# Kernel optimization log

Measured on AMD Instinct MI355X. Metric: run time of the kernel, lower is better.

## Reference

```python
import jax, jax.numpy as jnp
import numpy as np

H = 768  # sparse grid height
W = 768  # sparse grid width
N = 200000  # active sites
CIN = 256
CB = 64


def setup_inputs() -> dict:
    key = jax.random.key(0)
    ks = jax.random.split(key, 11)
    rng = np.random.default_rng(0)
    # unique active-site linear coordinates on the HxW grid
    coords = jnp.asarray(np.sort(rng.choice(H * W, N, replace=False)).astype(np.int64))
    feats = jax.random.normal(ks[0], (N, CIN), jnp.float32)
    w1 = jax.random.normal(ks[1], (CIN, CB), jnp.float32) / np.float32(np.sqrt(CIN))
    w2 = jax.random.normal(ks[2], (9, CB, CB), jnp.float32) / np.float32(np.sqrt(9 * CB))
    w3 = jax.random.normal(ks[3], (CB, CIN), jnp.float32) / np.float32(np.sqrt(CB))
    s1 = jax.random.uniform(ks[4], (CB,), jnp.float32, 0.5, 1.5)
    b1 = jax.random.normal(ks[5], (CB,), jnp.float32) * 0.1
    s2 = jax.random.uniform(ks[6], (CB,), jnp.float32, 0.5, 1.5)
    b2 = jax.random.normal(ks[7], (CB,), jnp.float32) * 0.1
    s3 = jax.random.uniform(ks[8], (CIN,), jnp.float32, 0.5, 1.5)
    b3 = jax.random.normal(ks[9], (CIN,), jnp.float32) * 0.1
    return dict(feats=feats, coords=coords, w1=w1, w2=w2, w3=w3,
                s1=s1, b1=b1, s2=s2, b2=b2, s3=s3, b3=b3)


def sparse_conv3x3(feats, coords, w2):
    # active-site sparse 3x3 conv: gather valid neighbors, matmul per tap, accumulate
    idx_map = jnp.full((H * W,), -1, jnp.int32).at[coords].set(
        jnp.arange(N, dtype=jnp.int32))
    y, x = coords // W, coords % W
    out = jnp.zeros((N, w2.shape[2]), feats.dtype)
    k = 0
    for dy in (-1, 0, 1):
        for dx in (-1, 0, 1):
            ny, nx = y + dy, x + dx
            inb = (ny >= 0) & (ny < H) & (nx >= 0) & (nx < W)
            lin = jnp.clip(ny, 0, H - 1) * W + jnp.clip(nx, 0, W - 1)
            r = idx_map[lin]
            ok = inb & (r >= 0)
            g = jnp.where(ok[:, None], feats[jnp.maximum(r, 0)], 0.0)
            out = out + g @ w2[k]
            k += 1
    return out


def reference(feats, coords, w1, w2, w3, s1, b1, s2, b2, s3, b3):
    identity = feats
    out = jax.nn.relu((feats @ w1) * s1 + b1)            # conv1 1x1 + bn1 + relu
    out = jax.nn.relu(sparse_conv3x3(out, coords, w2) * s2 + b2)  # conv2 3x3 + bn2 + relu
    out = (out @ w3) * s3 + b3                            # conv3 1x1 + bn3
    return jax.nn.relu(out + identity)                    # residual + relu
```

## Files before the change

### kernel.cpp

```cpp
#include <hip/hip_runtime.h>
#include <hip/hip_bf16.h>
#include <stdint.h>

#define HH 768
#define WW 768
#define NN 200000
#define CI 256
#define CB 64

typedef __attribute__((ext_vector_type(8))) __bf16 bf16x8;
typedef __attribute__((ext_vector_type(4))) float f32x4;
typedef __attribute__((ext_vector_type(4))) unsigned short u16x4;

__device__ inline unsigned short f2bf(float f) {
    union { float f; unsigned int i; } v; v.f = f;
    unsigned int r = v.i + 0x7FFF + ((v.i >> 16) & 1);
    return (unsigned short)(r >> 16);
}
__device__ inline f32x4 mfma16(bf16x8 a, bf16x8 b, f32x4 c) {
    return __builtin_amdgcn_mfma_f32_16x16x32_bf16(a, b, c, 0, 0, 0);
}
__device__ inline bf16x8 ldfrag(const unsigned short* p) {
    return *(const bf16x8*)p;
}
__device__ inline bf16x8 ldfrag_f32(const float* p) {
    float4 f0 = *(const float4*)(p);
    float4 f1 = *(const float4*)(p + 4);
    bf16x8 a;
    a[0] = (__bf16)f0.x; a[1] = (__bf16)f0.y; a[2] = (__bf16)f0.z; a[3] = (__bf16)f0.w;
    a[4] = (__bf16)f1.x; a[5] = (__bf16)f1.y; a[6] = (__bf16)f1.z; a[7] = (__bf16)f1.w;
    return a;
}


__global__ void k_scatter(const int* __restrict__ coords, int* __restrict__ idx_map) {
    int i = blockIdx.x * 256 + threadIdx.x;
    if (i < NN) idx_map[coords[i]] = i;
}

__global__ void k_prepw(const float* __restrict__ w1,
                        const float* __restrict__ w2,
                        const float* __restrict__ w3,
                        unsigned short* __restrict__ w1t,
                        unsigned short* __restrict__ w2t,
                        unsigned short* __restrict__ w3t) {
    int tid = blockIdx.x * 256 + threadIdx.x;
    int stride = gridDim.x * 256;
    for (int i = tid; i < CI * CB; i += stride) {
        int k = i / CB, n = i % CB;
        w1t[n * CI + k] = f2bf(w1[i]);
    }
    for (int i = tid; i < 9 * CB * CB; i += stride) {
        int t = i / (CB * CB), rem = i % (CB * CB);
        int k = rem / CB, n = rem % CB;
        w2t[t * CB * CB + n * CB + k] = f2bf(w2[i]);
    }
    for (int i = tid; i < CB * CI; i += stride) {
        int k = i / CI, n = i % CI;
        w3t[n * CB + k] = f2bf(w3[i]);
    }
}


__global__ __launch_bounds__(256, 4) void k_gemm1(const float* __restrict__ feats,
                                                  const unsigned short* __restrict__ w1t,
                                                  const float* __restrict__ s1,
                                                  const float* __restrict__ b1,
                                                  unsigned short* __restrict__ out1) {
    const int wave = threadIdx.x >> 6;
    const int lane = threadIdx.x & 63;
    const int m = lane & 15;
    const int quad = lane >> 4;
    const int row0 = blockIdx.x * 128 + wave * 32;
    if (row0 >= NN) return;

    f32x4 acc[2][4];
#pragma unroll
    for (int rt = 0; rt < 2; ++rt)
#pragma unroll
        for (int ct = 0; ct < 4; ++ct) acc[rt][ct] = (f32x4){0.f, 0.f, 0.f, 0.f};

#pragma unroll
    for (int ks = 0; ks < 8; ++ks) {
        bf16x8 f[2];
#pragma unroll
        for (int rt = 0; rt < 2; ++rt)
            f[rt] = ldfrag_f32(feats + (size_t)(row0 + rt * 16 + m) * CI + quad * 8 + ks * 32);
#pragma unroll
        for (int ct = 0; ct < 4; ++ct) {
            bf16x8 b = ldfrag(w1t + (ct * 16 + m) * CI + quad * 8 + ks * 32);
#pragma unroll
            for (int rt = 0; rt < 2; ++rt)
                acc[rt][ct] = mfma16(b, f[rt], acc[rt][ct]);
        }
    }

#pragma unroll
    for (int rt = 0; rt < 2; ++rt)
#pragma unroll
        for (int ct = 0; ct < 4; ++ct) {
            int row = row0 + rt * 16 + m;
            int c0 = ct * 16 + quad * 4;
            float4 sc = *(const float4*)(s1 + c0);
            float4 bi = *(const float4*)(b1 + c0);
            float v0 = acc[rt][ct][0] * sc.x + bi.x;
            float v1 = acc[rt][ct][1] * sc.y + bi.y;
            float v2 = acc[rt][ct][2] * sc.z + bi.z;
            float v3 = acc[rt][ct][3] * sc.w + bi.w;
            u16x4 o;
            o.x = f2bf(v0 > 0.f ? v0 : 0.f);
            o.y = f2bf(v1 > 0.f ? v1 : 0.f);
            o.z = f2bf(v2 > 0.f ? v2 : 0.f);
            o.w = f2bf(v3 > 0.f ? v3 : 0.f);
            *(u16x4*)(out1 + (size_t)row * CB + c0) = o;
        }
}


__global__ __launch_bounds__(256, 4) void k_conv(const unsigned short* __restrict__ out1,
                                                 const unsigned short* __restrict__ w2t,
                                                 const int* __restrict__ coords,
                                                 const int* __restrict__ idx_map,
                                                 const float* __restrict__ s2,
                                                 const float* __restrict__ b2,
                                                 const unsigned short* __restrict__ zrow,
                                                 unsigned short* __restrict__ out2) {
    __shared__ int s_nbr[128 * 9];
    const int tid = threadIdx.x;
    if (tid < 128) {
        int grow = blockIdx.x * 128 + tid;
        if (grow < NN) {
            int c = coords[grow];
            int y = c / WW, x = c - y * WW;
#pragma unroll
            for (int t = 0; t < 9; ++t) {
                int dy = t / 3 - 1, dx = t % 3 - 1;
                int ny = y + dy, nx = x + dx;
                int r = -1;
                if (ny >= 0 && ny < HH && nx >= 0 && nx < WW) r = idx_map[ny * WW + nx];
                s_nbr[tid * 9 + t] = r;
            }
        } else {
#pragma unroll
            for (int t = 0; t < 9; ++t) s_nbr[tid * 9 + t] = -1;
        }
    }
    __syncthreads();

    const int wave = tid >> 6;
    const int lane = tid & 63;
    const int m = lane & 15;
    const int quad = lane >> 4;
    const int row0 = blockIdx.x * 128 + wave * 32;
    if (row0 >= NN) return;

    f32x4 acc[2][4];
#pragma unroll
    for (int rt = 0; rt < 2; ++rt)
#pragma unroll
        for (int ct = 0; ct < 4; ++ct) acc[rt][ct] = (f32x4){0.f, 0.f, 0.f, 0.f};

#pragma unroll
    for (int t = 0; t < 9; ++t) {
        bf16x8 a[2][2];
#pragma unroll
        for (int rt = 0; rt < 2; ++rt) {
            int r = s_nbr[(wave * 32 + rt * 16 + m) * 9 + t];
            const unsigned short* base = (r >= 0) ? (out1 + (size_t)r * CB) : zrow;
            a[rt][0] = ldfrag(base + quad * 8);
            a[rt][1] = ldfrag(base + quad * 8 + 32);
        }
#pragma unroll
        for (int ks = 0; ks < 2; ++ks)
#pragma unroll
            for (int ct = 0; ct < 4; ++ct) {
                bf16x8 b = ldfrag(w2t + t * CB * CB + (ct * 16 + m) * CB + quad * 8 + ks * 32);
#pragma unroll
                for (int rt = 0; rt < 2; ++rt)
                    acc[rt][ct] = mfma16(b, a[rt][ks], acc[rt][ct]);
            }
    }

#pragma unroll
    for (int rt = 0; rt < 2; ++rt)
#pragma unroll
        for (int ct = 0; ct < 4; ++ct) {
            int row = row0 + rt * 16 + m;
            int c0 = ct * 16 + quad * 4;
            float4 sc = *(const float4*)(s2 + c0);
            float4 bi = *(const float4*)(b2 + c0);
            float v0 = acc[rt][ct][0] * sc.x + bi.x;
            float v1 = acc[rt][ct][1] * sc.y + bi.y;
            float v2 = acc[rt][ct][2] * sc.z + bi.z;
            float v3 = acc[rt][ct][3] * sc.w + bi.w;
            u16x4 o;
            o.x = f2bf(v0 > 0.f ? v0 : 0.f);
            o.y = f2bf(v1 > 0.f ? v1 : 0.f);
            o.z = f2bf(v2 > 0.f ? v2 : 0.f);
            o.w = f2bf(v3 > 0.f ? v3 : 0.f);
            *(u16x4*)(out2 + (size_t)row * CB + c0) = o;
        }
}


__global__ __launch_bounds__(256, 4) void k_gemm3(const unsigned short* __restrict__ out2,
                                                  const unsigned short* __restrict__ w3t,
                                                  const float* __restrict__ s3,
                                                  const float* __restrict__ b3,
                                                  const float* __restrict__ feats,
                                                  float* __restrict__ out) {
    const int wave = threadIdx.x >> 6;
    const int lane = threadIdx.x & 63;
    const int m = lane & 15;
    const int quad = lane >> 4;
    const int row0 = blockIdx.x * 128 + wave * 32;
    if (row0 >= NN) return;

    bf16x8 arow[2][2];
#pragma unroll
    for (int rt = 0; rt < 2; ++rt) {
        const unsigned short* ap = out2 + (size_t)(row0 + rt * 16 + m) * CB + quad * 8;
        arow[rt][0] = ldfrag(ap);
        arow[rt][1] = ldfrag(ap + 32);
    }

#pragma unroll
    for (int cc = 0; cc < 4; ++cc) {
        const int cbase = cc * 64;
        f32x4 acc[2][4];
#pragma unroll
        for (int rt = 0; rt < 2; ++rt)
#pragma unroll
            for (int ct = 0; ct < 4; ++ct) acc[rt][ct] = (f32x4){0.f, 0.f, 0.f, 0.f};

#pragma unroll
        for (int ks = 0; ks < 2; ++ks)
#pragma unroll
            for (int ct = 0; ct < 4; ++ct) {
                bf16x8 b = ldfrag(w3t + (cbase + ct * 16 + m) * CB + quad * 8 + ks * 32);
#pragma unroll
                for (int rt = 0; rt < 2; ++rt)
                    acc[rt][ct] = mfma16(b, arow[rt][ks], acc[rt][ct]);
            }

#pragma unroll
        for (int rt = 0; rt < 2; ++rt)
#pragma unroll
            for (int ct = 0; ct < 4; ++ct) {
                int row = row0 + rt * 16 + m;
                int c0 = cbase + ct * 16 + quad * 4;
                float4 sc = *(const float4*)(s3 + c0);
                float4 bi = *(const float4*)(b3 + c0);
                float4 fr = *(const float4*)(feats + (size_t)row * CI + c0);
                float4 v;
                v.x = acc[rt][ct][0] * sc.x + bi.x + fr.x;
                v.y = acc[rt][ct][1] * sc.y + bi.y + fr.y;
                v.z = acc[rt][ct][2] * sc.z + bi.z + fr.z;
                v.w = acc[rt][ct][3] * sc.w + bi.w + fr.w;
                v.x = v.x > 0.f ? v.x : 0.f;
                v.y = v.y > 0.f ? v.y : 0.f;
                v.z = v.z > 0.f ? v.z : 0.f;
                v.w = v.w > 0.f ? v.w : 0.f;
                *(float4*)(out + (size_t)row * CI + c0) = v;
            }
    }
}


extern "C" void kernel_launch(void* const* d_in, const int* in_sizes, int n_in,
                              void* d_out, int out_size, void* d_ws, size_t ws_size,
                              hipStream_t stream) {
    const float* feats = (const float*)d_in[0];
    const int* coords = (const int*)d_in[1];
    const float* w1 = (const float*)d_in[2];
    const float* w2 = (const float*)d_in[3];
    const float* w3 = (const float*)d_in[4];
    const float* s1 = (const float*)d_in[5];
    const float* b1 = (const float*)d_in[6];
    const float* s2 = (const float*)d_in[7];
    const float* b2 = (const float*)d_in[8];
    const float* s3 = (const float*)d_in[9];
    const float* b3 = (const float*)d_in[10];
    float* out = (float*)d_out;

    char* ws = (char*)d_ws;
    int* idx_map        = (int*)(ws + 0);
    unsigned short* w1t = (unsigned short*)(ws + 2359296);
    unsigned short* w2t = (unsigned short*)(ws + 2392064);
    unsigned short* w3t = (unsigned short*)(ws + 2465792);
    unsigned short* out1= (unsigned short*)(ws + 2498560);
    unsigned short* out2= (unsigned short*)(ws + 28098560);
    unsigned short* zrow= (unsigned short*)(ws + 53698560);

    hipMemsetAsync(idx_map, 0xFF, (size_t)HH * WW * 4, stream);
    hipMemsetAsync(zrow, 0x00, 128, stream);
    k_scatter<<<(NN + 255) / 256, 256, 0, stream>>>(coords, idx_map);
    k_prepw<<<64, 256, 0, stream>>>(w1, w2, w3, w1t, w2t, w3t);
    k_gemm1<<<(NN + 127) / 128, 256, 0, stream>>>(feats, w1t, s1, b1, out1);
    k_conv<<<(NN + 127) / 128, 256, 0, stream>>>(out1, w2t, coords, idx_map, s2, b2, zrow, out2);
    k_gemm3<<<(NN + 127) / 128, 256, 0, stream>>>(out2, w3t, s3, b3, feats, out);
}
```

Baseline: 582.1 us.

## Fuse sparse 3x3 conv with conv3 epilogue and prefetch residual feats

Merges the sparse conv kernel and the final 1x1 GEMM into one kernel. The bf16 conv output stays in per-wave shared memory instead of going out to global memory and coming back. Residual feature loads are double-buffered in registers, with the next column chunk prefetched while the current one is computed. This removes one kernel launch and the out2 round trip, but it raises register and LDS pressure, so the launch bound drops to 2 blocks per SM.

```diff
diff --git a/kernel.cpp b/kernel.cpp
--- a/kernel.cpp
+++ b/kernel.cpp
@@ -117,16 +117,39 @@
 }
 
 
-__global__ __launch_bounds__(256, 4) void k_conv(const unsigned short* __restrict__ out1,
-                                                 const unsigned short* __restrict__ w2t,
-                                                 const int* __restrict__ coords,
-                                                 const int* __restrict__ idx_map,
-                                                 const float* __restrict__ s2,
-                                                 const float* __restrict__ b2,
-                                                 const unsigned short* __restrict__ zrow,
-                                                 unsigned short* __restrict__ out2) {
+__global__ __launch_bounds__(256, 2) void k_conv3(const unsigned short* __restrict__ out1,
+                                                  const unsigned short* __restrict__ w2t,
+                                                  const unsigned short* __restrict__ w3t,
+                                                  const int* __restrict__ coords,
+                                                  const int* __restrict__ idx_map,
+                                                  const float* __restrict__ s2,
+                                                  const float* __restrict__ b2,
+                                                  const float* __restrict__ s3,
+                                                  const float* __restrict__ b3,
+                                                  const unsigned short* __restrict__ zrow,
+                                                  const float* __restrict__ feats,
+                                                  float* __restrict__ out) {
     __shared__ int s_nbr[128 * 9];
+    __shared__ unsigned short s_x[4][32][68];
+
     const int tid = threadIdx.x;
+    const int wave = tid >> 6;
+    const int lane = tid & 63;
+    const int m = lane & 15;
+    const int quad = lane >> 4;
+    const int row0 = blockIdx.x * 128 + wave * 32;
+    const bool live = (row0 < NN);
+
+    float4 fr[2][2][4];
+    if (live) {
+#pragma unroll
+        for (int rt = 0; rt < 2; ++rt)
+#pragma unroll
+            for (int ct = 0; ct < 4; ++ct)
+                fr[0][rt][ct] = *(const float4*)(feats + (size_t)(row0 + rt * 16 + m) * CI
+                                                 + ct * 16 + quad * 4);
+    }
+
     if (tid < 128) {
         int grow = blockIdx.x * 128 + tid;
         if (grow < NN) {
@@ -146,13 +169,7 @@
         }
     }
     __syncthreads();
-
-    const int wave = tid >> 6;
-    const int lane = tid & 63;
-    const int m = lane & 15;
-    const int quad = lane >> 4;
-    const int row0 = blockIdx.x * 128 + wave * 32;
-    if (row0 >= NN) return;
+    if (!live) return;
 
     f32x4 acc[2][4];
 #pragma unroll
@@ -185,7 +202,6 @@
     for (int rt = 0; rt < 2; ++rt)
 #pragma unroll
         for (int ct = 0; ct < 4; ++ct) {
-            int row = row0 + rt * 16 + m;
             int c0 = ct * 16 + quad * 4;
             float4 sc = *(const float4*)(s2 + c0);
             float4 bi = *(const float4*)(b2 + c0);
@@ -198,40 +214,34 @@
             o.y = f2bf(v1 > 0.f ? v1 : 0.f);
             o.z = f2bf(v2 > 0.f ? v2 : 0.f);
             o.w = f2bf(v3 > 0.f ? v3 : 0.f);
-            *(u16x4*)(out2 + (size_t)row * CB + c0) = o;
-        }
-}
-
-
-__global__ __launch_bounds__(256, 4) void k_gemm3(const unsigned short* __restrict__ out2,
-                                                  const unsigned short* __restrict__ w3t,
-                                                  const float* __restrict__ s3,
-                                                  const float* __restrict__ b3,
-                                                  const float* __restrict__ feats,
-                                                  float* __restrict__ out) {
-    const int wave = threadIdx.x >> 6;
-    const int lane = threadIdx.x & 63;
-    const int m = lane & 15;
-    const int quad = lane >> 4;
-    const int row0 = blockIdx.x * 128 + wave * 32;
-    if (row0 >= NN) return;
-
-    bf16x8 arow[2][2];
-#pragma unroll
-    for (int rt = 0; rt < 2; ++rt) {
-        const unsigned short* ap = out2 + (size_t)(row0 + rt * 16 + m) * CB + quad * 8;
-        arow[rt][0] = ldfrag(ap);
-        arow[rt][1] = ldfrag(ap + 32);
-    }
+            *(u16x4*)&s_x[wave][rt * 16 + m][c0] = o;
+        }
+
+    bf16x8 a3[2][2];
+#pragma unroll
+    for (int rt = 0; rt < 2; ++rt)
+#pragma unroll
+        for (int ks = 0; ks < 2; ++ks)
+            a3[rt][ks] = ldfrag(&s_x[wave][rt * 16 + m][ks * 32 + quad * 8]);
 
 #pragma unroll
     for (int cc = 0; cc < 4; ++cc) {
+        if (cc < 3) {
+#pragma unroll
+            for (int rt = 0; rt < 2; ++rt)
+#pragma unroll
+                for (int ct = 0; ct < 4; ++ct)
+                    fr[(cc + 1) & 1][rt][ct] =
+                        *(const float4*)(feats + (size_t)(row0 + rt * 16 + m) * CI
+                                         + (cc + 1) * 64 + ct * 16 + quad * 4);
+        }
+
         const int cbase = cc * 64;
-        f32x4 acc[2][4];
+        f32x4 acc3[2][4];
 #pragma unroll
         for (int rt = 0; rt < 2; ++rt)
 #pragma unroll
-            for (int ct = 0; ct < 4; ++ct) acc[rt][ct] = (f32x4){0.f, 0.f, 0.f, 0.f};
+            for (int ct = 0; ct < 4; ++ct) acc3[rt][ct] = (f32x4){0.f, 0.f, 0.f, 0.f};
 
 #pragma unroll
         for (int ks = 0; ks < 2; ++ks)
@@ -240,7 +250,7 @@
                 bf16x8 b = ldfrag(w3t + (cbase + ct * 16 + m) * CB + quad * 8 + ks * 32);
 #pragma unroll
                 for (int rt = 0; rt < 2; ++rt)
-                    acc[rt][ct] = mfma16(b, arow[rt][ks], acc[rt][ct]);
+                    acc3[rt][ct] = mfma16(b, a3[rt][ks], acc3[rt][ct]);
             }
 
 #pragma unroll
@@ -251,12 +261,12 @@
                 int c0 = cbase + ct * 16 + quad * 4;
                 float4 sc = *(const float4*)(s3 + c0);
                 float4 bi = *(const float4*)(b3 + c0);
-                float4 fr = *(const float4*)(feats + (size_t)row * CI + c0);
+                float4 f = fr[cc & 1][rt][ct];
                 float4 v;
-                v.x = acc[rt][ct][0] * sc.x + bi.x + fr.x;
-                v.y = acc[rt][ct][1] * sc.y + bi.y + fr.y;
-                v.z = acc[rt][ct][2] * sc.z + bi.z + fr.z;
-                v.w = acc[rt][ct][3] * sc.w + bi.w + fr.w;
+                v.x = acc3[rt][ct][0] * sc.x + bi.x + f.x;
+                v.y = acc3[rt][ct][1] * sc.y + bi.y + f.y;
+                v.z = acc3[rt][ct][2] * sc.z + bi.z + f.z;
+                v.w = acc3[rt][ct][3] * sc.w + bi.w + f.w;
                 v.x = v.x > 0.f ? v.x : 0.f;
                 v.y = v.y > 0.f ? v.y : 0.f;
                 v.z = v.z > 0.f ? v.z : 0.f;
@@ -289,7 +299,6 @@
     unsigned short* w2t = (unsigned short*)(ws + 2392064);
     unsigned short* w3t = (unsigned short*)(ws + 2465792);
     unsigned short* out1= (unsigned short*)(ws + 2498560);
-    unsigned short* out2= (unsigned short*)(ws + 28098560);
     unsigned short* zrow= (unsigned short*)(ws + 53698560);
 
     hipMemsetAsync(idx_map, 0xFF, (size_t)HH * WW * 4, stream);
@@ -297,6 +306,6 @@
     k_scatter<<<(NN + 255) / 256, 256, 0, stream>>>(coords, idx_map);
     k_prepw<<<64, 256, 0, stream>>>(w1, w2, w3, w1t, w2t, w3t);
     k_gemm1<<<(NN + 127) / 128, 256, 0, stream>>>(feats, w1t, s1, b1, out1);
-    k_conv<<<(NN + 127) / 128, 256, 0, stream>>>(out1, w2t, coords, idx_map, s2, b2, zrow, out2);
-    k_gemm3<<<(NN + 127) / 128, 256, 0, stream>>>(out2, w3t, s3, b3, feats, out);
-}
+    k_conv3<<<(NN + 127) / 128, 256, 0, stream>>>(out1, w2t, w3t, coords, idx_map,
+                                                  s2, b2, s3, b3, zrow, feats, out);
+}
```

Measured after the change: 535.7 us. 8.0% less time.
